# Kernel optimization log

Measured on AMD Instinct MI355X. Metric: run time of the kernel, lower is better.

The kernel has to match this reference:

```python
import jax, jax.numpy as jnp
import numpy as np

N, D, E, K = 32768, 256, 8, 2
H = 4 * D  # expert hidden dim


def setup_inputs() -> dict:
    key = jax.random.key(0)
    ks = jax.random.split(key, 8)
    s = 0.02
    return {
        "x": jax.random.normal(ks[0], (N, D), dtype=jnp.float32),
        "grad": jax.random.normal(ks[1], (N, 1), dtype=jnp.float32),
        "Wr": jax.random.normal(ks[2], (D + 1, E), dtype=jnp.float32) * s,
        "br": jnp.zeros((E,), dtype=jnp.float32),
        "W1": jax.random.normal(ks[3], (E, D, H), dtype=jnp.float32) * s,
        "b1": jnp.zeros((E, H), dtype=jnp.float32),
        "W2": jax.random.normal(ks[4], (E, H, D), dtype=jnp.float32) * s,
        "b2": jnp.zeros((E, D), dtype=jnp.float32),
    }


def reference(x, grad, Wr, br, W1, b1, W2, b2):
    # Router: softmax over experts on [x, grad] features
    router_in = jnp.concatenate([x, grad], axis=-1)          # [N, D+1]
    logits = router_in @ Wr + br                              # [N, E]
    probs = jax.nn.softmax(logits, axis=-1)
    topk_probs, topk_idx = jax.lax.top_k(probs, K)            # [N, K]
    # Combine weights: w[n, e] = topk prob if expert e selected for token n else 0
    combine = jnp.zeros_like(probs).at[
        jnp.arange(x.shape[0])[:, None], topk_idx
    ].add(topk_probs)                                         # [N, E]
    # Expert MLPs (dropout is identity in eval mode). Loop over small fixed E.
    out = jnp.zeros_like(x)
    for e in range(E):
        h = jax.nn.gelu(x @ W1[e] + b1[e], approximate=False)  # [N, H]
        y = h @ W2[e] + b2[e]                                  # [N, D]
        out = out + combine[:, e:e + 1] * y
    return out, probs
```

## Files before the change

kernel.cpp:

```cpp
#include <hip/hip_runtime.h>
#include <hip/hip_bf16.h>
#include <cmath>

#define N_TOK 32768
#define DIM   256
#define NEXP  8
#define HID   1024
#define BM    64
#define BH    64
#define MAXT  512

typedef short bf16x8 __attribute__((ext_vector_type(8)));
typedef float f32x4  __attribute__((ext_vector_type(4)));

__device__ __forceinline__ ushort f2bf(float f) {
  unsigned u = __builtin_bit_cast(unsigned, f);
  u += 0x7fffu + ((u >> 16) & 1u);
  return (ushort)(u >> 16);
}

__device__ __forceinline__ float gelu_f(float v) {
  float z  = 0.70710678118654752f * v;
  float az = fabsf(z);
  float t  = 1.0f / (1.0f + 0.3275911f * az);
  float y  = 1.0f - t*(0.254829592f + t*(-0.284496736f + t*(1.421413741f
                 + t*(-1.453152027f + t*1.061405429f)))) * __expf(-az*az);
  float er = (z < 0.f) ? -y : y;
  return 0.5f * v * (1.0f + er);
}

__device__ __forceinline__ int lh_slot(int row) {
  return ((row ^ (row >> 3)) & 7) << 4;
}
__device__ __forceinline__ int lx_slot(int row) {
  return (row & 7) << 4;
}

__global__ __launch_bounds__(256) void k_transpose_cast(
    const float* __restrict__ src, ushort* __restrict__ dst, int R, int C)
{
  __shared__ float tile[32][33];
  int e = blockIdx.z, rb = blockIdx.y, cb = blockIdx.x;
  int tx = threadIdx.x, ty = threadIdx.y;
  const float* s = src + (size_t)e * R * C;
  ushort* d = dst + (size_t)e * R * C;
#pragma unroll
  for (int j = 0; j < 4; ++j)
    tile[ty + 8*j][tx] = s[(size_t)(rb*32 + ty + 8*j) * C + cb*32 + tx];
  __syncthreads();
#pragma unroll
  for (int j = 0; j < 4; ++j)
    d[(size_t)(cb*32 + ty + 8*j) * R + rb*32 + tx] = f2bf(tile[tx][ty + 8*j]);
}

__global__ __launch_bounds__(256) void k_router(
    const float* __restrict__ x, const float* __restrict__ grad,
    const float* __restrict__ Wr, const float* __restrict__ br,
    float* __restrict__ probs_out,
    int* __restrict__ cnt, int* __restrict__ tok, float* __restrict__ wgt)
{
  __shared__ float xt[256][33];
  __shared__ float wrs[257*8];
  __shared__ float brs[8];
  __shared__ int lcnt[8], lbase[8];
  int tid = threadIdx.x;
  int n = blockIdx.x * 256 + tid;

  for (int i = tid; i < 257*8; i += 256) wrs[i] = Wr[i];
  if (tid < 8) { brs[tid] = br[tid]; lcnt[tid] = 0; }

  double acc[8] = {0,0,0,0,0,0,0,0};
  for (int ch = 0; ch < 8; ++ch) {
    __syncthreads();
    for (int f = tid; f < 2048; f += 256) {
      int r = f >> 3, c0 = (f & 7) * 4;
      float4 v = *(const float4*)(x + (size_t)(blockIdx.x*256 + r)*DIM + ch*32 + c0);
      xt[r][c0] = v.x; xt[r][c0+1] = v.y; xt[r][c0+2] = v.z; xt[r][c0+3] = v.w;
    }
    __syncthreads();
#pragma unroll 4
    for (int c = 0; c < 32; ++c) {
      double xv = (double)xt[tid][c];
      const float* wr = &wrs[(ch*32 + c)*8];
#pragma unroll
      for (int e = 0; e < 8; ++e) acc[e] += xv * (double)wr[e];
    }
  }
  double g = (double)grad[n];
  double lg[8];
#pragma unroll
  for (int e = 0; e < 8; ++e) lg[e] = acc[e] + g*(double)wrs[256*8+e] + (double)brs[e];
  double m = lg[0];
#pragma unroll
  for (int e = 1; e < 8; ++e) m = lg[e] > m ? lg[e] : m;
  double p[8], s = 0.0;
#pragma unroll
  for (int e = 0; e < 8; ++e) { p[e] = exp(lg[e]-m); s += p[e]; }
  double inv = 1.0/s;
#pragma unroll
  for (int e = 0; e < 8; ++e) probs_out[(size_t)n*8 + e] = (float)(p[e]*inv);

  int i0 = 0;
#pragma unroll
  for (int e = 1; e < 8; ++e) if (lg[e] > lg[i0]) i0 = e;
  int i1 = (i0 == 0) ? 1 : 0;
#pragma unroll
  for (int e = 0; e < 8; ++e) if (e != i0 && lg[e] > lg[i1]) i1 = e;
  float w0 = (float)(p[i0]*inv), w1 = (float)(p[i1]*inv);

  int p0 = atomicAdd(&lcnt[i0], 1);
  int p1 = atomicAdd(&lcnt[i1], 1);
  __syncthreads();
  if (tid < 8) lbase[tid] = atomicAdd(&cnt[tid], lcnt[tid]);
  __syncthreads();
  tok[i0*N_TOK + lbase[i0] + p0] = n;  wgt[i0*N_TOK + lbase[i0] + p0] = w0;
  tok[i1*N_TOK + lbase[i1] + p1] = n;  wgt[i1*N_TOK + lbase[i1] + p1] = w1;
}

__global__ __launch_bounds__(256, 2) void k_moe(
    const float* __restrict__ x,
    const ushort* __restrict__ w1t,
    const ushort* __restrict__ w2t,
    const float* __restrict__ bias1,
    const float* __restrict__ bias2,
    const int* __restrict__ cnt, const int* __restrict__ tok,
    const float* __restrict__ wgt,
    float* __restrict__ out)
{
  int e    = blockIdx.x & 7;
  int tile = blockIdx.x >> 3;
  int c = cnt[e];
  int row0 = tile * BM;
  if (row0 >= c) return;
  int rows = min(BM, c - row0);
  int phase = tile & 15;

  __shared__ ushort lx[BM * DIM];
  __shared__ ushort w1l[BH * DIM];
  __shared__ ushort lh[BM * BH];
  __shared__ float  lb1[HID];

  int tid  = threadIdx.x;
  int lane = tid & 63;
  int wid  = tid >> 6;
  const int l15 = lane & 15;
  const int lk8 = (lane >> 4) * 8;
  const int lr4 = (lane >> 4) * 4;
  const int wr = wid >> 1, wc = wid & 1;

  const int*   etok = tok + e * N_TOK + row0;
  const float* ewgt = wgt + e * N_TOK + row0;
  const ushort* W1e = w1t + (size_t)e * HID * DIM;
  const ushort* W2e = w2t + (size_t)e * DIM * HID;

  for (int f = tid; f < BM * (DIM/4); f += 256) {
    int r = f >> 6, c4 = f & 63;
    int t = etok[min(r, rows - 1)];
    float4 v = *(const float4*)(x + (size_t)t * DIM + c4 * 4);
    ushort4 b;
    b.x = f2bf(v.x); b.y = f2bf(v.y); b.z = f2bf(v.z); b.w = f2bf(v.w);
    *(ushort4*)((char*)lx + r * 512 + ((c4 * 8) ^ lx_slot(r))) = b;
  }
#pragma unroll
  for (int i = 0; i < 4; ++i) lb1[i*256 + tid] = bias1[e*HID + i*256 + tid];
  {
    int h0 = ((0 + phase) & 15) * BH;
#pragma unroll
    for (int i = 0; i < 8; ++i) {
      int u = i*256 + tid;
      int r = u >> 5, s = u & 31;
      const ushort* g = W1e + (size_t)(h0 + r) * DIM + ((s ^ (r & 7)) * 8);
      __builtin_amdgcn_global_load_lds(
          (const __attribute__((address_space(1))) unsigned int*)g,
          (__attribute__((address_space(3))) unsigned int*)(w1l + u*8),
          16, 0, 0);
    }
  }
  __syncthreads();

  bf16x8 areg[2][8];
#pragma unroll
  for (int fr = 0; fr < 2; ++fr) {
    int row = wr*32 + fr*16 + l15;
#pragma unroll
    for (int k = 0; k < 8; ++k)
      areg[fr][k] = *(const bf16x8*)((const char*)lx + row*512
                      + (((k*32 + lk8)*2) ^ lx_slot(row)));
  }

  f32x4 accY[4][4];
#pragma unroll
  for (int i = 0; i < 4; ++i)
#pragma unroll
    for (int j = 0; j < 4; ++j) accY[i][j] = (f32x4){0.f,0.f,0.f,0.f};

  int sl2[4];
#pragma unroll
  for (int fr = 0; fr < 4; ++fr) sl2[fr] = lh_slot(fr*16 + l15);

  const int b0row = wc*32 + l15;
  const int bxor  = (b0row & 7);

  for (int cc = 0; cc < HID / BH; ++cc) {
    int chunk = (cc + phase) & 15;
    int h0 = chunk * BH;

    bf16x8 bw[2][4];
#pragma unroll
    for (int k2 = 0; k2 < 2; ++k2)
#pragma unroll
      for (int fc = 0; fc < 4; ++fc)
        bw[k2][fc] = *(const bf16x8*)(W2e + (size_t)(wid*64 + fc*16 + l15) * HID
                                      + h0 + k2*32 + lk8);

    f32x4 accH[2][2];
#pragma unroll
    for (int i = 0; i < 2; ++i)
#pragma unroll
      for (int j = 0; j < 2; ++j) accH[i][j] = (f32x4){0.f,0.f,0.f,0.f};

#pragma unroll
    for (int k = 0; k < 8; ++k) {
      int s = k*4 + (lane >> 4);
      bf16x8 b0 = *(const bf16x8*)(w1l + ((b0row     )*32 + (s ^ bxor))*8);
      bf16x8 b1 = *(const bf16x8*)(w1l + ((b0row + 16)*32 + (s ^ bxor))*8);
      accH[0][0] = __builtin_amdgcn_mfma_f32_16x16x32_bf16(areg[0][k], b0, accH[0][0], 0, 0, 0);
      accH[1][0] = __builtin_amdgcn_mfma_f32_16x16x32_bf16(areg[1][k], b0, accH[1][0], 0, 0, 0);
      accH[0][1] = __builtin_amdgcn_mfma_f32_16x16x32_bf16(areg[0][k], b1, accH[0][1], 0, 0, 0);
      accH[1][1] = __builtin_amdgcn_mfma_f32_16x16x32_bf16(areg[1][k], b1, accH[1][1], 0, 0, 0);
    }

#pragma unroll
    for (int fc = 0; fc < 2; ++fc) {
      int col = wc*32 + fc*16 + l15;
      float bv = lb1[h0 + col];
#pragma unroll
      for (int fr = 0; fr < 2; ++fr)
#pragma unroll
        for (int j = 0; j < 4; ++j) {
          int row = wr*32 + fr*16 + lr4 + j;
          float v = gelu_f(accH[fr][fc][j] + bv);
          *(ushort*)((char*)lh + row*128 + ((col*2) ^ lh_slot(row))) = f2bf(v);
        }
    }
    __syncthreads();

    if (cc < HID/BH - 1) {
      int nh0 = ((cc + 1 + phase) & 15) * BH;
#pragma unroll
      for (int i = 0; i < 8; ++i) {
        int u = i*256 + tid;
        int r = u >> 5, s = u & 31;
        const ushort* g = W1e + (size_t)(nh0 + r) * DIM + ((s ^ (r & 7)) * 8);
        __builtin_amdgcn_global_load_lds(
            (const __attribute__((address_space(1))) unsigned int*)g,
            (__attribute__((address_space(3))) unsigned int*)(w1l + u*8),
            16, 0, 0);
      }
    }

#pragma unroll
    for (int k2 = 0; k2 < 2; ++k2) {
      bf16x8 a2[4];
#pragma unroll
      for (int fr = 0; fr < 4; ++fr) {
        int row = fr*16 + l15;
        a2[fr] = *(const bf16x8*)((const char*)lh + row*128 + (((k2*32 + lk8)*2) ^ sl2[fr]));
      }
#pragma unroll
      for (int fr = 0; fr < 4; ++fr)
#pragma unroll
        for (int fc = 0; fc < 4; ++fc)
          accY[fr][fc] = __builtin_amdgcn_mfma_f32_16x16x32_bf16(a2[fr], bw[k2][fc], accY[fr][fc], 0, 0, 0);
    }
    __syncthreads();
  }

  float b2v[4];
#pragma unroll
  for (int fc = 0; fc < 4; ++fc) b2v[fc] = bias2[e*DIM + wid*64 + fc*16 + l15];
#pragma unroll
  for (int fr = 0; fr < 4; ++fr) {
#pragma unroll
    for (int j = 0; j < 4; ++j) {
      int r = fr*16 + lr4 + j;
      if (r < rows) {
        int t = etok[r];
        float w = ewgt[r];
#pragma unroll
        for (int fc = 0; fc < 4; ++fc)
          atomicAdd(out + (size_t)t * DIM + wid*64 + fc*16 + l15,
                    w * (accY[fr][fc][j] + b2v[fc]));
      }
    }
  }
}

extern "C" void kernel_launch(void* const* d_in, const int* in_sizes, int n_in,
                              void* d_out, int out_size, void* d_ws, size_t ws_size,
                              hipStream_t stream)
{
  const float* x    = (const float*)d_in[0];
  const float* grad = (const float*)d_in[1];
  const float* Wr   = (const float*)d_in[2];
  const float* br   = (const float*)d_in[3];
  const float* W1   = (const float*)d_in[4];
  const float* b1   = (const float*)d_in[5];
  const float* W2   = (const float*)d_in[6];
  const float* b2   = (const float*)d_in[7];
  float* out   = (float*)d_out;
  float* probs = out + (size_t)N_TOK * DIM;

  char* wsb = (char*)d_ws;
  int*    cnt = (int*)wsb;
  int*    tok = (int*)   (wsb + 4096);
  float*  wgt = (float*) (wsb + 4096 + (size_t)NEXP*N_TOK*4);
  ushort* w1t = (ushort*)(wsb + 4096 + (size_t)NEXP*N_TOK*8);
  ushort* w2t = w1t + (size_t)NEXP * HID * DIM;

  hipMemsetAsync(d_out, 0, (size_t)N_TOK * DIM * sizeof(float), stream);
  hipMemsetAsync(cnt, 0, NEXP * sizeof(int), stream);

  k_transpose_cast<<<dim3(HID/32, DIM/32, NEXP), dim3(32, 8), 0, stream>>>(W1, w1t, DIM, HID);
  k_transpose_cast<<<dim3(DIM/32, HID/32, NEXP), dim3(32, 8), 0, stream>>>(W2, w2t, HID, DIM);
  k_router<<<N_TOK/256, 256, 0, stream>>>(x, grad, Wr, br, probs, cnt, tok, wgt);
  k_moe<<<NEXP*MAXT, 256, 0, stream>>>(x, w1t, w2t, b1, b2, cnt, tok, wgt, out);
}
```

Before: 260.2 us.

## Double-buffer W1 chunks in LDS and replace output atomics with slab plus combine

The W1 chunk buffer now alternates with the x staging buffer: x is loaded into registers, then the LDS region is reused so the next W1 chunk can be prefetched before the current chunk's GEMM, removing one barrier's worth of exposed latency per chunk. The router tags each token's second expert assignment with a high bit. When the workspace is large enough, the MoE kernel writes the first-choice result directly to out and the second-choice result to a separate slab, and a new elementwise kernel sums them. This replaces scattered float atomics with plain stores, at the cost of an extra 32 MB read-modify-write pass and a dependence on workspace size. The output memset stays in place.

Measured after the change: 236.9 us. -9.0%, faster.

```diff
diff --git a/kernel.cpp b/kernel.cpp
--- a/kernel.cpp
+++ b/kernel.cpp
@@ -113,10 +113,11 @@
   __syncthreads();
   if (tid < 8) lbase[tid] = atomicAdd(&cnt[tid], lcnt[tid]);
   __syncthreads();
-  tok[i0*N_TOK + lbase[i0] + p0] = n;  wgt[i0*N_TOK + lbase[i0] + p0] = w0;
-  tok[i1*N_TOK + lbase[i1] + p1] = n;  wgt[i1*N_TOK + lbase[i1] + p1] = w1;
-}
-
+  tok[i0*N_TOK + lbase[i0] + p0] = n;              wgt[i0*N_TOK + lbase[i0] + p0] = w0;
+  tok[i1*N_TOK + lbase[i1] + p1] = n | (1 << 30);  wgt[i1*N_TOK + lbase[i1] + p1] = w1;
+}
+
+template<int SLAB>
 __global__ __launch_bounds__(256, 2) void k_moe(
     const float* __restrict__ x,
     const ushort* __restrict__ w1t,
@@ -125,7 +126,7 @@
     const float* __restrict__ bias2,
     const int* __restrict__ cnt, const int* __restrict__ tok,
     const float* __restrict__ wgt,
-    float* __restrict__ out)
+    float* __restrict__ out, float* __restrict__ slab)
 {
   int e    = blockIdx.x & 7;
   int tile = blockIdx.x >> 3;
@@ -135,8 +136,8 @@
   int rows = min(BM, c - row0);
   int phase = tile & 15;
 
-  __shared__ ushort lx[BM * DIM];
-  __shared__ ushort w1l[BH * DIM];
+  __shared__ ushort lsA[BM * DIM];
+  __shared__ ushort lsB[BH * DIM];
   __shared__ ushort lh[BM * BH];
   __shared__ float  lb1[HID];
 
@@ -155,16 +156,16 @@
 
   for (int f = tid; f < BM * (DIM/4); f += 256) {
     int r = f >> 6, c4 = f & 63;
-    int t = etok[min(r, rows - 1)];
+    int t = etok[min(r, rows - 1)] & 0xFFFF;
     float4 v = *(const float4*)(x + (size_t)t * DIM + c4 * 4);
     ushort4 b;
     b.x = f2bf(v.x); b.y = f2bf(v.y); b.z = f2bf(v.z); b.w = f2bf(v.w);
-    *(ushort4*)((char*)lx + r * 512 + ((c4 * 8) ^ lx_slot(r))) = b;
+    *(ushort4*)((char*)lsA + r * 512 + ((c4 * 8) ^ lx_slot(r))) = b;
   }
 #pragma unroll
   for (int i = 0; i < 4; ++i) lb1[i*256 + tid] = bias1[e*HID + i*256 + tid];
   {
-    int h0 = ((0 + phase) & 15) * BH;
+    int h0 = (phase & 15) * BH;
 #pragma unroll
     for (int i = 0; i < 8; ++i) {
       int u = i*256 + tid;
@@ -172,7 +173,7 @@
       const ushort* g = W1e + (size_t)(h0 + r) * DIM + ((s ^ (r & 7)) * 8);
       __builtin_amdgcn_global_load_lds(
           (const __attribute__((address_space(1))) unsigned int*)g,
-          (__attribute__((address_space(3))) unsigned int*)(w1l + u*8),
+          (__attribute__((address_space(3))) unsigned int*)(lsB + u*8),
           16, 0, 0);
     }
   }
@@ -184,9 +185,10 @@
     int row = wr*32 + fr*16 + l15;
 #pragma unroll
     for (int k = 0; k < 8; ++k)
-      areg[fr][k] = *(const bf16x8*)((const char*)lx + row*512
+      areg[fr][k] = *(const bf16x8*)((const char*)lsA + row*512
                       + (((k*32 + lk8)*2) ^ lx_slot(row)));
   }
+  __syncthreads();
 
   f32x4 accY[4][4];
 #pragma unroll
@@ -204,46 +206,8 @@
   for (int cc = 0; cc < HID / BH; ++cc) {
     int chunk = (cc + phase) & 15;
     int h0 = chunk * BH;
-
-    bf16x8 bw[2][4];
-#pragma unroll
-    for (int k2 = 0; k2 < 2; ++k2)
-#pragma unroll
-      for (int fc = 0; fc < 4; ++fc)
-        bw[k2][fc] = *(const bf16x8*)(W2e + (size_t)(wid*64 + fc*16 + l15) * HID
-                                      + h0 + k2*32 + lk8);
-
-    f32x4 accH[2][2];
-#pragma unroll
-    for (int i = 0; i < 2; ++i)
-#pragma unroll
-      for (int j = 0; j < 2; ++j) accH[i][j] = (f32x4){0.f,0.f,0.f,0.f};
-
-#pragma unroll
-    for (int k = 0; k < 8; ++k) {
-      int s = k*4 + (lane >> 4);
-      bf16x8 b0 = *(const bf16x8*)(w1l + ((b0row     )*32 + (s ^ bxor))*8);
-      bf16x8 b1 = *(const bf16x8*)(w1l + ((b0row + 16)*32 + (s ^ bxor))*8);
-      accH[0][0] = __builtin_amdgcn_mfma_f32_16x16x32_bf16(areg[0][k], b0, accH[0][0], 0, 0, 0);
-      accH[1][0] = __builtin_amdgcn_mfma_f32_16x16x32_bf16(areg[1][k], b0, accH[1][0], 0, 0, 0);
-      accH[0][1] = __builtin_amdgcn_mfma_f32_16x16x32_bf16(areg[0][k], b1, accH[0][1], 0, 0, 0);
-      accH[1][1] = __builtin_amdgcn_mfma_f32_16x16x32_bf16(areg[1][k], b1, accH[1][1], 0, 0, 0);
-    }
-
-#pragma unroll
-    for (int fc = 0; fc < 2; ++fc) {
-      int col = wc*32 + fc*16 + l15;
-      float bv = lb1[h0 + col];
-#pragma unroll
-      for (int fr = 0; fr < 2; ++fr)
-#pragma unroll
-        for (int j = 0; j < 4; ++j) {
-          int row = wr*32 + fr*16 + lr4 + j;
-          float v = gelu_f(accH[fr][fc][j] + bv);
-          *(ushort*)((char*)lh + row*128 + ((col*2) ^ lh_slot(row))) = f2bf(v);
-        }
-    }
-    __syncthreads();
+    ushort* cur = (cc & 1) ? lsA : lsB;
+    ushort* nxt = (cc & 1) ? lsB : lsA;
 
     if (cc < HID/BH - 1) {
       int nh0 = ((cc + 1 + phase) & 15) * BH;
@@ -254,10 +218,50 @@
         const ushort* g = W1e + (size_t)(nh0 + r) * DIM + ((s ^ (r & 7)) * 8);
         __builtin_amdgcn_global_load_lds(
             (const __attribute__((address_space(1))) unsigned int*)g,
-            (__attribute__((address_space(3))) unsigned int*)(w1l + u*8),
+            (__attribute__((address_space(3))) unsigned int*)(nxt + u*8),
             16, 0, 0);
       }
     }
+
+    bf16x8 bw[2][4];
+#pragma unroll
+    for (int k2 = 0; k2 < 2; ++k2)
+#pragma unroll
+      for (int fc = 0; fc < 4; ++fc)
+        bw[k2][fc] = *(const bf16x8*)(W2e + (size_t)(wid*64 + fc*16 + l15) * HID
+                                      + h0 + k2*32 + lk8);
+
+    f32x4 accH[2][2];
+#pragma unroll
+    for (int i = 0; i < 2; ++i)
+#pragma unroll
+      for (int j = 0; j < 2; ++j) accH[i][j] = (f32x4){0.f,0.f,0.f,0.f};
+
+#pragma unroll
+    for (int k = 0; k < 8; ++k) {
+      int s = k*4 + (lane >> 4);
+      bf16x8 b0 = *(const bf16x8*)(cur + ((b0row     )*32 + (s ^ bxor))*8);
+      bf16x8 b1 = *(const bf16x8*)(cur + ((b0row + 16)*32 + (s ^ bxor))*8);
+      accH[0][0] = __builtin_amdgcn_mfma_f32_16x16x32_bf16(areg[0][k], b0, accH[0][0], 0, 0, 0);
+      accH[1][0] = __builtin_amdgcn_mfma_f32_16x16x32_bf16(areg[1][k], b0, accH[1][0], 0, 0, 0);
+      accH[0][1] = __builtin_amdgcn_mfma_f32_16x16x32_bf16(areg[0][k], b1, accH[0][1], 0, 0, 0);
+      accH[1][1] = __builtin_amdgcn_mfma_f32_16x16x32_bf16(areg[1][k], b1, accH[1][1], 0, 0, 0);
+    }
+
+#pragma unroll
+    for (int fc = 0; fc < 2; ++fc) {
+      int col = wc*32 + fc*16 + l15;
+      float bv = lb1[h0 + col];
+#pragma unroll
+      for (int fr = 0; fr < 2; ++fr)
+#pragma unroll
+        for (int j = 0; j < 4; ++j) {
+          int row = wr*32 + fr*16 + lr4 + j;
+          float v = gelu_f(accH[fr][fc][j] + bv);
+          *(ushort*)((char*)lh + row*128 + ((col*2) ^ lh_slot(row))) = f2bf(v);
+        }
+    }
+    __syncthreads();
 
 #pragma unroll
     for (int k2 = 0; k2 < 2; ++k2) {
@@ -285,14 +289,35 @@
     for (int j = 0; j < 4; ++j) {
       int r = fr*16 + lr4 + j;
       if (r < rows) {
-        int t = etok[r];
+        int raw = etok[r];
+        int t   = raw & 0xFFFF;
         float w = ewgt[r];
-#pragma unroll
-        for (int fc = 0; fc < 4; ++fc)
-          atomicAdd(out + (size_t)t * DIM + wid*64 + fc*16 + l15,
-                    w * (accY[fr][fc][j] + b2v[fc]));
+        if (SLAB) {
+          float* dst = ((raw >> 30) ? slab : out) + (size_t)t * DIM;
+#pragma unroll
+          for (int fc = 0; fc < 4; ++fc)
+            dst[wid*64 + fc*16 + l15] = w * (accY[fr][fc][j] + b2v[fc]);
+        } else {
+#pragma unroll
+          for (int fc = 0; fc < 4; ++fc)
+            atomicAdd(out + (size_t)t * DIM + wid*64 + fc*16 + l15,
+                      w * (accY[fr][fc][j] + b2v[fc]));
+        }
       }
     }
+  }
+}
+
+__global__ __launch_bounds__(256) void k_combine(
+    float* __restrict__ out, const float* __restrict__ slab)
+{
+  int stride = gridDim.x * blockDim.x;
+  for (int i = blockIdx.x * blockDim.x + threadIdx.x;
+       i < N_TOK * DIM / 4; i += stride) {
+    float4 a = ((const float4*)out)[i];
+    float4 b = ((const float4*)slab)[i];
+    a.x += b.x; a.y += b.y; a.z += b.z; a.w += b.w;
+    ((float4*)out)[i] = a;
   }
 }
 
@@ -317,6 +342,9 @@
   float*  wgt = (float*) (wsb + 4096 + (size_t)NEXP*N_TOK*4);
   ushort* w1t = (ushort*)(wsb + 4096 + (size_t)NEXP*N_TOK*8);
   ushort* w2t = w1t + (size_t)NEXP * HID * DIM;
+  float*  slab = (float*)(wsb + (size_t)(16 << 20));
+
+  bool use_slab = ws_size >= ((size_t)(16 << 20) + (size_t)N_TOK * DIM * 4);
 
   hipMemsetAsync(d_out, 0, (size_t)N_TOK * DIM * sizeof(float), stream);
   hipMemsetAsync(cnt, 0, NEXP * sizeof(int), stream);
@@ -324,5 +352,10 @@
   k_transpose_cast<<<dim3(HID/32, DIM/32, NEXP), dim3(32, 8), 0, stream>>>(W1, w1t, DIM, HID);
   k_transpose_cast<<<dim3(DIM/32, HID/32, NEXP), dim3(32, 8), 0, stream>>>(W2, w2t, HID, DIM);
   k_router<<<N_TOK/256, 256, 0, stream>>>(x, grad, Wr, br, probs, cnt, tok, wgt);
-  k_moe<<<NEXP*MAXT, 256, 0, stream>>>(x, w1t, w2t, b1, b2, cnt, tok, wgt, out);
-}
+  if (use_slab) {
+    k_moe<1><<<NEXP*MAXT, 256, 0, stream>>>(x, w1t, w2t, b1, b2, cnt, tok, wgt, out, slab);
+    k_combine<<<2048, 256, 0, stream>>>(out, slab);
+  } else {
+    k_moe<0><<<NEXP*MAXT, 256, 0, stream>>>(x, w1t, w2t, b1, b2, cnt, tok, wgt, out, slab);
+  }
+}
```
